# Performance work log

Measured on AMD Instinct MI355X. Metric: run time of the kernel, lower is better.

## Reference

```python
import jax, jax.numpy as jnp
import numpy as np

B, T, DIM, HEADS, DH, MLP = 2, 1024, 768, 8, 96, 3072
EPS = 1e-6


def _rms_norm(x, w):
    return x * jax.lax.rsqrt(jnp.mean(x * x, axis=-1, keepdims=True) + EPS) * w


def _rotate_half(x):
    x1, x2 = jnp.split(x, 2, axis=-1)
    return jnp.concatenate([-x2, x1], axis=-1)


def _l2norm(x):
    n = jnp.sqrt(jnp.sum(x * x, axis=-1, keepdims=True))
    return x / jnp.maximum(n, 1e-12)


def setup_inputs() -> dict:
    key = jax.random.key(0)
    ks = jax.random.split(key, 16)
    def rn(k, shape, s=0.02):
        return jax.random.normal(k, shape, jnp.float32) * s
    return {
        'x_stream1': jax.random.normal(ks[0], (B, T, DIM), jnp.float32),
        'x_stream2': jax.random.normal(ks[1], (B, T, DIM), jnp.float32),
        'p_emb': jax.random.normal(ks[2], (B, 1, 1024), jnp.float32),
        'mod_w1': rn(ks[3], (1024, 512)), 'mod_b1': jnp.zeros((512,), jnp.float32),
        'mod_w2': rn(ks[4], (512, DIM * 12)), 'mod_b2': jnp.zeros((DIM * 12,), jnp.float32),
        'norm11_w': jnp.ones((DIM,), jnp.float32), 'norm12_w': jnp.ones((DIM,), jnp.float32),
        'qkv_w': rn(ks[5], (DIM, 3 * DIM)), 'qkv_b': jnp.zeros((3 * DIM,), jnp.float32),
        'qkv2_w': rn(ks[6], (DIM, 3 * DIM)), 'qkv2_b': jnp.zeros((3 * DIM,), jnp.float32),
        'qk_scale': jnp.full((DH,), 10.0, jnp.float32),
        'out_w': rn(ks[7], (DIM, DIM)), 'out_b': jnp.zeros((DIM,), jnp.float32),
        'norm21_w': jnp.ones((DIM,), jnp.float32), 'norm22_w': jnp.ones((DIM,), jnp.float32),
        'mlp1_w1': rn(ks[8], (DIM, MLP)), 'mlp1_b1': jnp.zeros((MLP,), jnp.float32),
        'mlp1_w2': rn(ks[9], (MLP, DIM)), 'mlp1_b2': jnp.zeros((DIM,), jnp.float32),
        'mlp2_w1': rn(ks[10], (DIM, MLP)), 'mlp2_b1': jnp.zeros((MLP,), jnp.float32),
        'mlp2_w2': rn(ks[11], (MLP, DIM)), 'mlp2_b2': jnp.zeros((DIM,), jnp.float32),
    }


def _forward(x_stream1, x_stream2, p_emb, mod_w1, mod_b1, mod_w2, mod_b2,
             norm11_w, norm12_w, qkv_w, qkv_b, qkv2_w, qkv2_b, qk_scale,
             out_w, out_b, norm21_w, norm22_w,
             mlp1_w1, mlp1_b1, mlp1_w2, mlp1_b2,
             mlp2_w1, mlp2_b1, mlp2_w2, mlp2_b2):
    Bc, Tc, D = x_stream1.shape
    # modulation MLP: SiLU -> Linear -> SiLU -> Linear -> 12 chunks of [B, D]
    h = jax.nn.silu(p_emb[:, 0, :])
    h = jax.nn.silu(h @ mod_w1 + mod_b1)
    mod = h @ mod_w2 + mod_b2
    (m1s, m1h, m1g, m2s, m2h, m2g,
     m3s, m3h, m3g, m4s, m4h, m4g) = [m[:, None, :] for m in jnp.split(mod, 12, axis=1)]

    xm1 = _rms_norm(x_stream1, norm11_w) * (1 + m1s) + m1h
    xm2 = _rms_norm(x_stream2, norm12_w) * (1 + m2s) + m2h

    q1, k1, v1 = jnp.split(xm1 @ qkv_w + qkv_b, 3, axis=-1)
    q2, k2, v2 = jnp.split(xm2 @ qkv2_w + qkv2_b, 3, axis=-1)
    q = jnp.concatenate([q1, q2], axis=1)  # [B, 2T, D]
    k = jnp.concatenate([k1, k2], axis=1)
    v = jnp.concatenate([v1, v2], axis=1)
    N = 2 * Tc

    def to_heads(x):
        return x.reshape(Bc, N, HEADS, DH).transpose(0, 2, 1, 3)  # [B, H, N, dh]
    q, k, v = to_heads(q), to_heads(k), to_heads(v)

    # RoPE (inv_freq computed in bf16 as in the original, then used in fp32)
    inv_freq = (1.0 / (10000.0 ** (jnp.arange(0, DH, 2, dtype=jnp.float32) / DH))).astype(jnp.bfloat16).astype(jnp.float32)
    t = jnp.arange(N, dtype=jnp.float32)
    freqs = t[:, None] * inv_freq[None, :]
    emb = jnp.concatenate([freqs, freqs], axis=-1)  # [N, dh]
    cos, sin = jnp.cos(emb), jnp.sin(emb)
    q = q * cos + _rotate_half(q) * sin
    k = k * cos + _rotate_half(k) * sin

    # QK-Norm
    q = _l2norm(q) * qk_scale
    k = _l2norm(k) * qk_scale

    scores = jnp.einsum('bhid,bhjd->bhij', q, k) * (DH ** -0.5)
    probs = jax.nn.softmax(scores, axis=-1)
    attn = jnp.einsum('bhij,bhjd->bhid', probs, v)
    attn = attn.transpose(0, 2, 1, 3).reshape(Bc, N, D)
    attn = attn @ out_w + out_b

    x1 = x_stream1 + attn[:, :Tc, :] * m1g
    x2 = x_stream2 + attn[:, Tc:, :] * m2g

    xn1 = _rms_norm(x1, norm21_w) * (1 + m3s) + m3h
    mlp1 = jax.nn.gelu(xn1 @ mlp1_w1 + mlp1_b1, approximate=False) @ mlp1_w2 + mlp1_b2
    xn2 = _rms_norm(x2, norm22_w) * (1 + m4s) + m4h
    mlp2 = jax.nn.gelu(xn2 @ mlp2_w1 + mlp2_b1, approximate=False) @ mlp2_w2 + mlp2_b2

    return (x1 + mlp1 * m3g, x2 + mlp2 * m4g)


def reference(x_stream1, x_stream2, p_emb, mod_w1, mod_b1, mod_w2, mod_b2,
              norm11_w, norm12_w, qkv_w, qkv_b, qkv2_w, qkv2_b, qk_scale,
              out_w, out_b, norm21_w, norm22_w,
              mlp1_w1, mlp1_b1, mlp1_w2, mlp1_b2,
              mlp2_w1, mlp2_b1, mlp2_w2, mlp2_b2):
    return _forward(x_stream1, x_stream2, p_emb, mod_w1, mod_b1, mod_w2, mod_b2,
                    norm11_w, norm12_w, qkv_w, qkv_b, qkv2_w, qkv2_b, qk_scale,
                    out_w, out_b, norm21_w, norm22_w,
                    mlp1_w1, mlp1_b1, mlp1_w2, mlp1_b2,
                    mlp2_w1, mlp2_b1, mlp2_w2, mlp2_b2)
```

## Files before the change

### kernel.cpp

```cpp
#include <hip/hip_runtime.h>
#include <hip/hip_bf16.h>
#include <cstdint>
#include <math.h>

#define BB 2
#define TT 1024
#define DIMM 768
#define NHEADS 8
#define DHH 96
#define MLPD 3072
#define NN 2048

typedef unsigned short u16;
using short8 = __attribute__((ext_vector_type(8))) short;
using f32x4  = __attribute__((ext_vector_type(4))) float;
using f32x16 = __attribute__((ext_vector_type(16))) float;
using int4v  = __attribute__((ext_vector_type(4))) int;
union S8I4 { int4v i; short8 s; };

static constexpr float kEps = 1e-6f;

__device__ __forceinline__ float siluf(float x){ return x / (1.f + expf(-x)); }
__device__ __forceinline__ float geluf(float x){ return 0.5f*x*(1.f + erff(x*0.7071067811865475f)); }
__device__ __forceinline__ float bf16_rne(float x){
  uint32_t u = __float_as_uint(x);
  u = (u + 0x7fffu + ((u >> 16) & 1u)) & 0xffff0000u;
  return __uint_as_float(u);
}
__device__ __forceinline__ u16 f2b(float x){
  uint32_t u = __float_as_uint(x);
  return (u16)((u + 0x7fffu + ((u >> 16) & 1u)) >> 16);
}
__device__ __forceinline__ float b2f(u16 b){
  return __uint_as_float(((uint32_t)b) << 16);
}
__device__ __forceinline__ int cvtpk(float lo, float hi){
  int d; asm("v_cvt_pk_bf16_f32 %0, %1, %2" : "=v"(d) : "v"(lo), "v"(hi)); return d;
}
__device__ __forceinline__ void gload16(const void* g, void* l){
  __builtin_amdgcn_global_load_lds((const __attribute__((address_space(1))) unsigned int*)g,
                                   (__attribute__((address_space(3))) unsigned int*)l, 16, 0, 0);
}

__global__ __launch_bounds__(256) void mod_stage1_k(
    const float* __restrict__ p_emb, const float* __restrict__ w1,
    const float* __restrict__ b1, float* __restrict__ h2){
  __shared__ float sp[1024];
  const int b = blockIdx.x >> 1;
  const int obase = (blockIdx.x & 1) * 256;
  for (int i = threadIdx.x; i < 1024; i += 256)
    sp[i] = siluf(p_emb[b*1024 + i]);
  __syncthreads();
  const int o = obase + threadIdx.x;
  float acc = 0.f;
  for (int j = 0; j < 1024; ++j) acc += sp[j] * w1[j*512 + o];
  h2[b*512 + o] = siluf(acc + b1[o]);
}

__global__ __launch_bounds__(256) void mod_stage2_k(
    const float* __restrict__ h2, const float* __restrict__ w2,
    const float* __restrict__ b2, float* __restrict__ mod){
  __shared__ float sh[512];
  const int b = blockIdx.x / 36;
  const int obase = (blockIdx.x % 36) * 256;
  for (int i = threadIdx.x; i < 512; i += 256)
    sh[i] = h2[b*512 + i];
  __syncthreads();
  const int o = obase + threadIdx.x;
  float acc = 0.f;
  for (int j = 0; j < 512; ++j) acc += sh[j] * w2[j*9216 + o];
  mod[b*9216 + o] = acc + b2[o];
}

__global__ __launch_bounds__(256) void wt_all_k(
    const float* __restrict__ s0, u16* __restrict__ d0,
    const float* __restrict__ s1, u16* __restrict__ d1,
    const float* __restrict__ s2, u16* __restrict__ d2,
    const float* __restrict__ s3, u16* __restrict__ d3,
    const float* __restrict__ s4, u16* __restrict__ d4,
    const float* __restrict__ s5, u16* __restrict__ d5,
    const float* __restrict__ s6, u16* __restrict__ d6){
  const int bid = blockIdx.x;
  const float* S; u16* D; int K, N, lid;
  if      (bid < 1728) { S=s0; D=d0; K=768;  N=2304; lid=bid; }
  else if (bid < 3456) { S=s1; D=d1; K=768;  N=2304; lid=bid-1728; }
  else if (bid < 4032) { S=s2; D=d2; K=768;  N=768;  lid=bid-3456; }
  else if (bid < 6336) { S=s3; D=d3; K=768;  N=3072; lid=bid-4032; }
  else if (bid < 8640) { S=s4; D=d4; K=3072; N=768;  lid=bid-6336; }
  else if (bid < 10944){ S=s5; D=d5; K=768;  N=3072; lid=bid-8640; }
  else                 { S=s6; D=d6; K=3072; N=768;  lid=bid-10944; }
  const int nx = N >> 5;
  const int k0 = (lid / nx) * 32, n0 = (lid % nx) * 32;
  __shared__ float t[32][33];
  const int tx = threadIdx.x & 31, ty = threadIdx.x >> 5;
  for (int i = ty; i < 32; i += 8)
    t[i][tx] = S[(size_t)(k0+i)*N + n0 + tx];
  __syncthreads();
  for (int i = ty; i < 32; i += 8)
    D[(size_t)(n0+i)*K + k0 + tx] = f2b(t[tx][i]);
}

__global__ __launch_bounds__(256) void rmsnorm2_k(
    const float* __restrict__ x0, const float* __restrict__ w0, int cs0, int ch0, u16* __restrict__ o0,
    const float* __restrict__ x1, const float* __restrict__ w1, int cs1, int ch1, u16* __restrict__ o1,
    const float* __restrict__ mod){
  const int rowg = blockIdx.x;
  const int s = rowg >> 11;
  const int row = rowg & 2047;
  const float* x = s ? x1 : x0;
  const float* w = s ? w1 : w0;
  const int cs = s ? cs1 : cs0, ch = s ? ch1 : ch0;
  u16* out = s ? o1 : o0;
  const int b = row >> 10;
  const int tid = threadIdx.x;
  const float* xr = x + (size_t)row * DIMM;
  float v0 = xr[tid], v1 = xr[tid + 256], v2 = xr[tid + 512];
  float ss = v0*v0 + v1*v1 + v2*v2;
  __shared__ float red[4];
  for (int m = 1; m < 64; m <<= 1) ss += __shfl_xor(ss, m, 64);
  if ((tid & 63) == 0) red[tid >> 6] = ss;
  __syncthreads();
  float tot = red[0] + red[1] + red[2] + red[3];
  float rms = rsqrtf(tot * (1.f/768.f) + kEps);
  const float* ms = mod + (size_t)b*9216 + (size_t)cs*768;
  const float* mh = mod + (size_t)b*9216 + (size_t)ch*768;
  u16* orow = out + (size_t)row * DIMM;
  orow[tid]       = f2b(v0*rms*w[tid]      *(1.f+ms[tid])       + mh[tid]);
  orow[tid + 256] = f2b(v1*rms*w[tid+256]  *(1.f+ms[tid+256])   + mh[tid+256]);
  orow[tid + 512] = f2b(v2*rms*w[tid+512]  *(1.f+ms[tid+512])   + mh[tid+512]);
}

template<int EPI, int DUAL>
__global__ __launch_bounds__(256) void gemm_pipe_k(
    const u16* __restrict__ A0, const u16* __restrict__ Bt0,
    const float* __restrict__ bias0, void* __restrict__ C0,
    const u16* __restrict__ A1, const u16* __restrict__ Bt1,
    const float* __restrict__ bias1, void* __restrict__ C1,
    int M, int N, int K){
  __shared__ u16 As[3][128*32];
  __shared__ u16 Bs[3][128*32];
  const int z = DUAL ? blockIdx.z : 0;
  const u16* A      = z ? A1 : A0;
  const u16* Bt     = z ? Bt1 : Bt0;
  const float* bias = z ? bias1 : bias0;
  void* C           = z ? C1 : C0;
  const int tid = threadIdx.x;
  const int w = tid >> 6, l = tid & 63;
  const int m0 = blockIdx.y*128, n0 = blockIdx.x*128;
  const int wr = w >> 1, wc = w & 1;
  const int la = l & 15, hi4 = l >> 4;
  f32x4 acc[4][4] = {};
  const int nk = K >> 5;
  const int sb0 = w*128, sb1 = w*128 + 64;
  const int s0i = sb0 + l, s1i = sb1 + l;
  const int r0 = s0i >> 2, c0 = ((s0i & 3) ^ ((r0 >> 1) & 3)) * 8;
  const int r1 = s1i >> 2, c1 = ((s1i & 3) ^ ((r1 >> 1) & 3)) * 8;
  const u16* Ar0 = A  + (size_t)(m0+r0)*K + c0;
  const u16* Ar1 = A  + (size_t)(m0+r1)*K + c1;
  const u16* Br0 = Bt + (size_t)(n0+r0)*K + c0;
  const u16* Br1 = Bt + (size_t)(n0+r1)*K + c1;
  #define STAGE(buf, kofs) { \
    gload16(Ar0 + (kofs), &As[buf][sb0*8]); \
    gload16(Br0 + (kofs), &Bs[buf][sb0*8]); \
    gload16(Ar1 + (kofs), &As[buf][sb1*8]); \
    gload16(Br1 + (kofs), &Bs[buf][sb1*8]); }
  STAGE(0, 0);
  STAGE(1, 32);
  const int rslot = ((hi4 ^ ((l >> 1) & 3)) << 4);
  int cur = 0;
  for (int kt = 0; kt < nk; ++kt){
    if (kt + 1 < nk){ asm volatile("s_waitcnt vmcnt(4)" ::: "memory"); }
    else            { asm volatile("s_waitcnt vmcnt(0)" ::: "memory"); }
    __builtin_amdgcn_s_barrier();
    if (kt + 2 < nk){
      int nb = cur + 2; if (nb >= 3) nb -= 3;
      STAGE(nb, (kt+2) << 5);
    }
    short8 af[4], bf[4];
    #pragma unroll
    for (int mi = 0; mi < 4; ++mi)
      af[mi] = *(const short8*)((const char*)&As[cur][0] + (wr*64 + mi*16 + la)*64 + rslot);
    #pragma unroll
    for (int ni = 0; ni < 4; ++ni)
      bf[ni] = *(const short8*)((const char*)&Bs[cur][0] + (wc*64 + ni*16 + la)*64 + rslot);
    #pragma unroll
    for (int mi = 0; mi < 4; ++mi)
      #pragma unroll
      for (int ni = 0; ni < 4; ++ni)
        acc[mi][ni] = __builtin_amdgcn_mfma_f32_16x16x32_bf16(af[mi], bf[ni], acc[mi][ni], 0, 0, 0);
    if (++cur == 3) cur = 0;
  }
  #undef STAGE
  #pragma unroll
  for (int mi = 0; mi < 4; ++mi){
    #pragma unroll
    for (int ni = 0; ni < 4; ++ni){
      const int n = n0 + wc*64 + ni*16 + la;
      const float bv = bias[n];
      #pragma unroll
      for (int rr = 0; rr < 4; ++rr){
        const int m = m0 + wr*64 + mi*16 + hi4*4 + rr;
        float v = acc[mi][ni][rr] + bv;
        if constexpr (EPI == 2) v = geluf(v);
        ((u16*)C)[(size_t)m*N + n] = f2b(v);
      }
    }
  }
}

template<int EPI, int DUAL>
__global__ __launch_bounds__(1024) void gemm16_k(
    const u16* __restrict__ A0, const u16* __restrict__ Bt0,
    const float* __restrict__ bias0,
    const u16* __restrict__ A1, const u16* __restrict__ Bt1,
    const float* __restrict__ bias1,
    const float* __restrict__ mod, const float* __restrict__ X0,
    const float* __restrict__ X1, float* __restrict__ O0,
    float* __restrict__ O1, int cg0, int cg1,
    int M, int N, int K){
  __shared__ char lds[131072];
  const int bid = blockIdx.x;
  const int xcd = bid & 7, kk = bid >> 3;
  const int g = xcd + 8*(kk/6);
  const int x = kk % 6;
  int by, z;
  if constexpr (DUAL){ by = g & 15; z = g >> 4; } else { by = g; z = 0; }
  const u16* A      = z ? A1 : A0;
  const u16* Bt     = z ? Bt1 : Bt0;
  const float* bias = z ? bias1 : bias0;
  const int tid = threadIdx.x;
  const int w = tid >> 6, l = tid & 63;
  const int kg = w >> 2, gw = w & 3;
  const int m0 = by*128, n0 = x*128;
  const int wr = gw >> 1, wc = gw & 1;
  const int la = l & 15, hi4 = l >> 4;
  u16* AsG = (u16*)(lds + kg*32768);
  u16* BsG = (u16*)(lds + kg*32768 + 16384);
  const int Kg = K >> 2;
  const int nk = Kg >> 5;
  const int kbase = kg * Kg;
  f32x4 acc[4][4] = {};
  #pragma unroll
  for (int it = 0; it < 2; ++it){
    const int sb = gw*128 + it*64;
    const int s = sb + l;
    const int row = s >> 2, scol = ((s & 3) ^ ((row >> 1) & 3)) * 8;
    gload16(A  + (size_t)(m0+row)*K + kbase + scol, AsG + sb*8);
    gload16(Bt + (size_t)(n0+row)*K + kbase + scol, BsG + sb*8);
  }
  __syncthreads();
  const int rslot = (hi4 ^ ((l >> 1) & 3)) * 8;
  for (int kt = 0; kt < nk; ++kt){
    const int cur = kt & 1;
    if (kt + 1 < nk){
      const int k0n = kbase + ((kt+1) << 5);
      #pragma unroll
      for (int it = 0; it < 2; ++it){
        const int sb = gw*128 + it*64;
        const int s = sb + l;
        const int row = s >> 2, scol = ((s & 3) ^ ((row >> 1) & 3)) * 8;
        gload16(A  + (size_t)(m0+row)*K + k0n + scol, AsG + (cur^1)*4096 + sb*8);
        gload16(Bt + (size_t)(n0+row)*K + k0n + scol, BsG + (cur^1)*4096 + sb*8);
      }
    }
    short8 af[4], bf[4];
    #pragma unroll
    for (int mi = 0; mi < 4; ++mi)
      af[mi] = *(const short8*)(AsG + cur*4096 + (wr*64 + mi*16 + la)*32 + rslot);
    #pragma unroll
    for (int ni = 0; ni < 4; ++ni)
      bf[ni] = *(const short8*)(BsG + cur*4096 + (wc*64 + ni*16 + la)*32 + rslot);
    #pragma unroll
    for (int mi = 0; mi < 4; ++mi)
      #pragma unroll
      for (int ni = 0; ni < 4; ++ni)
        acc[mi][ni] = __builtin_amdgcn_mfma_f32_16x16x32_bf16(af[mi], bf[ni], acc[mi][ni], 0, 0, 0);
    __syncthreads();
  }
  float* c0 = (float*)lds;
  float* c1 = (float*)(lds + 65536);
  #define WRACC(cb) { \
    _Pragma("unroll") for (int mi = 0; mi < 4; ++mi) \
    _Pragma("unroll") for (int ni = 0; ni < 4; ++ni) \
    _Pragma("unroll") for (int rr = 0; rr < 4; ++rr) \
      (cb)[(wr*64+mi*16+hi4*4+rr)*128 + wc*64+ni*16+la] = acc[mi][ni][rr]; }
  #define RDACC(cb) { \
    _Pragma("unroll") for (int mi = 0; mi < 4; ++mi) \
    _Pragma("unroll") for (int ni = 0; ni < 4; ++ni) \
    _Pragma("unroll") for (int rr = 0; rr < 4; ++rr) \
      acc[mi][ni][rr] += (cb)[(wr*64+mi*16+hi4*4+rr)*128 + wc*64+ni*16+la]; }
  if (kg == 1) WRACC(c0);
  if (kg == 3) WRACC(c1);
  __syncthreads();
  if (kg == 0) RDACC(c0);
  if (kg == 2) RDACC(c1);
  __syncthreads();
  if (kg == 2) WRACC(c0);
  __syncthreads();
  if (kg == 0){
    RDACC(c0);
    #pragma unroll
    for (int mi = 0; mi < 4; ++mi){
      #pragma unroll
      for (int ni = 0; ni < 4; ++ni){
        const int n = n0 + wc*64 + ni*16 + la;
        const float bv = bias[n];
        #pragma unroll
        for (int rr = 0; rr < 4; ++rr){
          const int m = m0 + wr*64 + mi*16 + hi4*4 + rr;
          float v = acc[mi][ni][rr] + bv;
          if constexpr (EPI == 3){
            const int bb = m >> 11, ss = (m >> 10) & 1, t = m & 1023;
            const float* X = ss ? X1 : X0;
            float* O = ss ? O1 : O0;
            const float gmod = mod[(size_t)bb*9216 + (size_t)(ss ? cg1 : cg0)*768 + n];
            const size_t oi = ((size_t)(bb*1024 + t))*768 + n;
            O[oi] = X[oi] + v*gmod;
          } else {
            float* O = z ? O1 : O0;
            const int cg = z ? cg1 : cg0;
            const int bb = m >> 10;
            const float gmod = mod[(size_t)bb*9216 + (size_t)cg*768 + n];
            O[(size_t)m*N + n] += v*gmod;
          }
        }
      }
    }
  }
  #undef WRACC
  #undef RDACC
}

__global__ __launch_bounds__(256) void build_qkv_k(
    const u16* __restrict__ qkv1, const u16* __restrict__ qkv2,
    const float* __restrict__ qk_scale,
    u16* __restrict__ Q, u16* __restrict__ K, u16* __restrict__ V){
  const int wid = threadIdx.x >> 6;
  const int lane = threadIdx.x & 63;
  const int row = blockIdx.x * 4 + wid;
  const int n = row & 2047;
  const int h = (row >> 11) & 7;
  const int b = row >> 14;
  const u16* src = (n < TT) ? (qkv1 + ((size_t)b*TT + n) * 2304)
                            : (qkv2 + ((size_t)b*TT + (n - TT)) * 2304);
  const int col = h * DHH;
  const bool act = lane < 48;
  float q0=0,q1=0,k0=0,k1=0,v0=0,v1=0,c=1.f,s=0.f,sc0=0,sc1=0;
  if (act){
    q0 = b2f(src[col + lane]);        q1 = b2f(src[col + lane + 48]);
    k0 = b2f(src[768 + col + lane]);  k1 = b2f(src[768 + col + lane + 48]);
    v0 = b2f(src[1536 + col + lane]); v1 = b2f(src[1536 + col + lane + 48]);
    float inv = bf16_rne((float)(1.0 / pow(10000.0, (2.0 * lane) / 96.0)));
    float ang = (float)n * inv;
    c = cosf(ang); s = sinf(ang);
    sc0 = qk_scale[lane]; sc1 = qk_scale[lane + 48];
  }
  float qr0 = q0*c - q1*s, qr1 = q1*c + q0*s;
  float kr0 = k0*c - k1*s, kr1 = k1*c + k0*s;
  float ssq = qr0*qr0 + qr1*qr1;
  float ssk = kr0*kr0 + kr1*kr1;
  for (int m = 1; m < 64; m <<= 1){ ssq += __shfl_xor(ssq, m, 64); ssk += __shfl_xor(ssk, m, 64); }
  float rq = 1.f / fmaxf(sqrtf(ssq), 1e-12f);
  float rk = 1.f / fmaxf(sqrtf(ssk), 1e-12f);
  const float sscale = 0.1020620726159658f;
  if (act){
    size_t base = (size_t)row * DHH;
    Q[base + lane]      = f2b(qr0*rq*sc0*sscale);  Q[base + lane + 48] = f2b(qr1*rq*sc1*sscale);
    K[base + lane]      = f2b(kr0*rk*sc0);         K[base + lane + 48] = f2b(kr1*rk*sc1);
    V[base + lane]      = f2b(v0);                 V[base + lane + 48] = f2b(v1);
  }
}

__global__ __launch_bounds__(256) void vtrans_k(
    const u16* __restrict__ Vtmp, u16* __restrict__ Vt){
  __shared__ u16 t[32][33];
  const int bh = blockIdx.z;
  const int n0 = blockIdx.x*32, d0 = blockIdx.y*32;
  const int tx = threadIdx.x & 31, ty = threadIdx.x >> 5;
  for (int i = ty; i < 32; i += 8)
    t[i][tx] = Vtmp[((size_t)bh*NN + n0+i)*DHH + d0 + tx];
  __syncthreads();
  for (int i = ty; i < 32; i += 8)
    Vt[((size_t)bh*DHH + d0+i)*NN + n0 + tx] = t[tx][i];
}

#define CROW(r) (((r)&3) + 8*((r)>>2) + 4*hi)
#define SMAXC 10.5f
#define BUILD_PA(dst, vec, basei) { \
  int a1_ = cvtpk(vec[basei+0], vec[basei+1]); \
  int b1_ = cvtpk(vec[basei+4], vec[basei+5]); \
  asm("v_permlane32_swap_b32 %0, %1" : "+v"(a1_), "+v"(b1_)); \
  int a2_ = cvtpk(vec[basei+2], vec[basei+3]); \
  int b2_ = cvtpk(vec[basei+6], vec[basei+7]); \
  asm("v_permlane32_swap_b32 %0, %1" : "+v"(a2_), "+v"(b2_)); \
  S8I4 u_; u_.i = (int4v){a1_, a2_, b1_, b2_}; dst = u_.s; }

__global__ __launch_bounds__(512) void attn_mfma_k(
    const u16* __restrict__ Qg, const u16* __restrict__ Kg,
    const u16* __restrict__ Vtg, u16* __restrict__ AO){
  __shared__ u16 Ks[2][2][64*128];
  __shared__ u16 Vs[2][2][96*64];
  const int bh = blockIdx.x >> 4;
  const int qblk = blockIdx.x & 15;
  const int b = bh >> 3, h = bh & 7;
  const int tid = threadIdx.x;
  const int w = tid >> 6, l = tid & 63;
  const int g2 = w >> 2, wq = w & 3;
  const int gtid = tid & 255;
  const int hi = l >> 5, li = l & 31;
  const int q0w = qblk*128 + wq*32;
  const int kvbase = g2 * 1024;

  short8 qf[6];
  {
    const u16* qrow = Qg + ((size_t)bh*NN + q0w + li)*DHH;
    #pragma unroll
    for (int ks = 0; ks < 6; ++ks)
      qf[ks] = *(const short8*)(qrow + ks*16 + hi*8);
  }

  f32x16 o0, o1, o2;
  #pragma unroll
  for (int r = 0; r < 16; ++r){ o0[r]=0.f; o1[r]=0.f; o2[r]=0.f; }
  float lrun = 0.f;

  {
    #pragma unroll
    for (int it = 0; it < 3; ++it){
      const int s = gtid + it*256;
      const int krow = s/12, ksl = s%12;
      short8 kv = *(const short8*)(Kg + ((size_t)bh*NN + kvbase + krow)*DHH + ksl*8);
      *(short8*)((char*)&Ks[g2][0][0] + krow*256 + ((ksl ^ (krow&7))<<4)) = kv;
      const int vrow = s >> 3, vsl = s & 7;
      short8 vv = *(const short8*)(Vtg + ((size_t)bh*DHH + vrow)*NN + kvbase + vsl*8);
      *(short8*)((char*)&Vs[g2][0][0] + vrow*128 + ((vsl ^ (vrow&7))<<4)) = vv;
    }
  }
  __syncthreads();

  const int NT2 = 16;
  for (int t = 0; t < NT2; ++t){
    const int cur = t & 1;
    short8 kst[3], vst[3];
    if (t + 1 < NT2){
      const int kv0 = kvbase + (t+1)*64;
      #pragma unroll
      for (int it = 0; it < 3; ++it){
        const int s = gtid + it*256;
        const int krow = s/12, ksl = s%12;
        kst[it] = *(const short8*)(Kg + ((size_t)bh*NN + kv0 + krow)*DHH + ksl*8);
        const int vrow = s >> 3, vsl = s & 7;
        vst[it] = *(const short8*)(Vtg + ((size_t)bh*DHH + vrow)*NN + kv0 + vsl*8);
      }
    }
    f32x16 s0, s1;
    #pragma unroll
    for (int r = 0; r < 16; ++r){ s0[r]=0.f; s1[r]=0.f; }
    #pragma unroll
    for (int ks = 0; ks < 6; ++ks){
      const int sl = ks*2 + hi;
      short8 kf0 = *(const short8*)((const char*)&Ks[g2][cur][0] + li*256      + ((sl ^ (li&7))<<4));
      short8 kf1 = *(const short8*)((const char*)&Ks[g2][cur][0] + (32+li)*256 + ((sl ^ ((32+li)&7))<<4));
      s0 = __builtin_amdgcn_mfma_f32_32x32x16_bf16(kf0, qf[ks], s0, 0, 0, 0);
      s1 = __builtin_amdgcn_mfma_f32_32x32x16_bf16(kf1, qf[ks], s1, 0, 0, 0);
    }
    float ps = 0.f;
    #pragma unroll
    for (int r = 0; r < 16; ++r){
      float pa = __expf(s0[r] - SMAXC);
      float pb = __expf(s1[r] - SMAXC);
      s0[r] = pa; s1[r] = pb; ps += pa + pb;
    }
    ps += __shfl_xor(ps, 32);
    lrun += ps;
    short8 pa0, pa1, pa2, pa3;
    BUILD_PA(pa0, s0, 0); BUILD_PA(pa1, s0, 8);
    BUILD_PA(pa2, s1, 0); BUILD_PA(pa3, s1, 8);
    #pragma unroll
    for (int dt = 0; dt < 3; ++dt){
      const int drow = dt*32 + li;
      const char* vb_base = (const char*)&Vs[g2][cur][0] + drow*128;
      f32x16* op = (dt==0)? &o0 : (dt==1)? &o1 : &o2;
      {
        short8 vb = *(const short8*)(vb_base + (((0*2+hi) ^ (drow&7))<<4));
        *op = __builtin_amdgcn_mfma_f32_32x32x16_bf16(pa0, vb, *op, 0, 0, 0);
      }
      {
        short8 vb = *(const short8*)(vb_base + (((1*2+hi) ^ (drow&7))<<4));
        *op = __builtin_amdgcn_mfma_f32_32x32x16_bf16(pa1, vb, *op, 0, 0, 0);
      }
      {
        short8 vb = *(const short8*)(vb_base + (((2*2+hi) ^ (drow&7))<<4));
        *op = __builtin_amdgcn_mfma_f32_32x32x16_bf16(pa2, vb, *op, 0, 0, 0);
      }
      {
        short8 vb = *(const short8*)(vb_base + (((3*2+hi) ^ (drow&7))<<4));
        *op = __builtin_amdgcn_mfma_f32_32x32x16_bf16(pa3, vb, *op, 0, 0, 0);
      }
    }
    __syncthreads();
    if (t + 1 < NT2){
      #pragma unroll
      for (int it = 0; it < 3; ++it){
        const int s = gtid + it*256;
        const int krow = s/12, ksl = s%12;
        *(short8*)((char*)&Ks[g2][cur^1][0] + krow*256 + ((ksl ^ (krow&7))<<4)) = kst[it];
        const int vrow = s >> 3, vsl = s & 7;
        *(short8*)((char*)&Vs[g2][cur^1][0] + vrow*128 + ((vsl ^ (vrow&7))<<4)) = vst[it];
      }
      __syncthreads();
    }
  }

  float* cmb = (float*)&Ks[0][0][0];
  float* cl  = (float*)&Vs[0][0][0];
  if (g2 == 1){
    #pragma unroll
    for (int r = 0; r < 16; ++r){
      cmb[((wq*16 + r)*3 + 0)*64 + l] = o0[r];
      cmb[((wq*16 + r)*3 + 1)*64 + l] = o1[r];
      cmb[((wq*16 + r)*3 + 2)*64 + l] = o2[r];
    }
    if (l < 32) cl[wq*32 + l] = lrun;
  }
  __syncthreads();
  if (g2 == 0){
    #pragma unroll
    for (int r = 0; r < 16; ++r){
      o0[r] += cmb[((wq*16 + r)*3 + 0)*64 + l];
      o1[r] += cmb[((wq*16 + r)*3 + 1)*64 + l];
      o2[r] += cmb[((wq*16 + r)*3 + 2)*64 + l];
    }
    lrun += cl[wq*32 + li];
    const float linv = 1.f / lrun;
    #pragma unroll
    for (int r = 0; r < 16; ++r){
      const float lr = __shfl(linv, CROW(r), 64);
      const int n = q0w + CROW(r);
      u16* dst = AO + ((size_t)b*NN + n)*DIMM + h*DHH + li;
      dst[0]  = f2b(o0[r]*lr);
      dst[32] = f2b(o1[r]*lr);
      dst[64] = f2b(o2[r]*lr);
    }
  }
}

static constexpr size_t W_QKV1T = 0;
static constexpr size_t W_QKV2T = W_QKV1T + 3538944;
static constexpr size_t W_OUTT  = W_QKV2T + 3538944;
static constexpr size_t W_M1W1T = W_OUTT  + 1179648;
static constexpr size_t W_M1W2T = W_M1W1T + 4718592;
static constexpr size_t W_M2W1T = W_M1W2T + 4718592;
static constexpr size_t W_M2W2T = W_M2W1T + 4718592;
static constexpr size_t O_MODH  = W_M2W2T + 4718592;
static constexpr size_t O_MODB  = O_MODH + 4096;
static constexpr size_t DYN     = O_MODB + 73728;
static constexpr size_t O_XM1   = DYN;
static constexpr size_t O_XM2   = O_XM1 + 3145728;
static constexpr size_t O_QKV1  = O_XM2 + 3145728;
static constexpr size_t O_QKV2  = O_QKV1 + 9437184;
static constexpr size_t O_QB    = O_QKV2 + 9437184;
static constexpr size_t O_KB    = O_QB + 6291456;
static constexpr size_t O_VTMP  = O_KB + 6291456;
static constexpr size_t O_PF    = O_VTMP + 6291456;
static constexpr size_t O_VT    = O_QKV1;
static constexpr size_t O_AO    = O_QKV2;
static constexpr size_t O_H1    = O_QB;
static constexpr size_t O_H2    = O_PF;

extern "C" void kernel_launch(void* const* d_in, const int* in_sizes, int n_in,
                              void* d_out, int out_size, void* d_ws, size_t ws_size,
                              hipStream_t stream){
  const float* x_s1   = (const float*)d_in[0];
  const float* x_s2   = (const float*)d_in[1];
  const float* p_emb  = (const float*)d_in[2];
  const float* mod_w1 = (const float*)d_in[3];
  const float* mod_b1 = (const float*)d_in[4];
  const float* mod_w2 = (const float*)d_in[5];
  const float* mod_b2 = (const float*)d_in[6];
  const float* n11_w  = (const float*)d_in[7];
  const float* n12_w  = (const float*)d_in[8];
  const float* qkv_w  = (const float*)d_in[9];
  const float* qkv_b  = (const float*)d_in[10];
  const float* qkv2_w = (const float*)d_in[11];
  const float* qkv2_b = (const float*)d_in[12];
  const float* qk_sc  = (const float*)d_in[13];
  const float* out_w  = (const float*)d_in[14];
  const float* out_b  = (const float*)d_in[15];
  const float* n21_w  = (const float*)d_in[16];
  const float* n22_w  = (const float*)d_in[17];
  const float* m1w1   = (const float*)d_in[18];
  const float* m1b1   = (const float*)d_in[19];
  const float* m1w2   = (const float*)d_in[20];
  const float* m1b2   = (const float*)d_in[21];
  const float* m2w1   = (const float*)d_in[22];
  const float* m2b1   = (const float*)d_in[23];
  const float* m2w2   = (const float*)d_in[24];
  const float* m2b2   = (const float*)d_in[25];

  char* ws = (char*)d_ws;
  u16* qkv1t = (u16*)(ws + W_QKV1T);
  u16* qkv2t = (u16*)(ws + W_QKV2T);
  u16* outt  = (u16*)(ws + W_OUTT);
  u16* w11t  = (u16*)(ws + W_M1W1T);
  u16* w12t  = (u16*)(ws + W_M1W2T);
  u16* w21t  = (u16*)(ws + W_M2W1T);
  u16* w22t  = (u16*)(ws + W_M2W2T);
  float* h2b  = (float*)(ws + O_MODH);
  float* modb = (float*)(ws + O_MODB);
  u16* xm1  = (u16*)(ws + O_XM1);
  u16* xm2  = (u16*)(ws + O_XM2);
  u16* qkv1 = (u16*)(ws + O_QKV1);
  u16* qkv2 = (u16*)(ws + O_QKV2);
  u16* Qb   = (u16*)(ws + O_QB);
  u16* Kb   = (u16*)(ws + O_KB);
  u16* Vtmp = (u16*)(ws + O_VTMP);
  u16* Vt   = (u16*)(ws + O_VT);
  u16* AO   = (u16*)(ws + O_AO);
  u16* H1   = (u16*)(ws + O_H1);
  u16* H2   = (u16*)(ws + O_H2);

  float* out0 = (float*)d_out;
  float* out1 = out0 + (size_t)BB*TT*DIMM;

  wt_all_k<<<13248, 256, 0, stream>>>(qkv_w, qkv1t, qkv2_w, qkv2t, out_w, outt,
                                      m1w1, w11t, m1w2, w12t, m2w1, w21t, m2w2, w22t);

  mod_stage1_k<<<4, 256, 0, stream>>>(p_emb, mod_w1, mod_b1, h2b);
  mod_stage2_k<<<72, 256, 0, stream>>>(h2b, mod_w2, mod_b2, modb);

  rmsnorm2_k<<<2*BB*TT, 256, 0, stream>>>(x_s1, n11_w, 0, 1, xm1,
                                          x_s2, n12_w, 3, 4, xm2, modb);

  gemm_pipe_k<1,1><<<dim3(18, 16, 2), 256, 0, stream>>>(
      xm1, qkv1t, qkv_b, qkv1, xm2, qkv2t, qkv2_b, qkv2, 2048, 2304, 768);

  build_qkv_k<<<(BB*NHEADS*NN)/4, 256, 0, stream>>>(qkv1, qkv2, qk_sc, Qb, Kb, Vtmp);

  vtrans_k<<<dim3(NN/32, DHH/32, 16), 256, 0, stream>>>(Vtmp, Vt);

  attn_mfma_k<<<16*16, 512, 0, stream>>>(Qb, Kb, Vt, AO);

  gemm16_k<3,0><<<192, 1024, 0, stream>>>(
      AO, outt, out_b, AO, outt, out_b,
      modb, x_s1, x_s2, out0, out1, 2, 5, 4096, 768, 768);

  rmsnorm2_k<<<2*BB*TT, 256, 0, stream>>>(out0, n21_w, 6, 7, xm1,
                                          out1, n22_w, 9, 10, xm2, modb);

  gemm_pipe_k<2,1><<<dim3(24, 16, 2), 256, 0, stream>>>(
      xm1, w11t, m1b1, H1, xm2, w21t, m2b1, H2, 2048, 3072, 768);

  gemm16_k<4,1><<<192, 1024, 0, stream>>>(
      H1, w12t, m1b2, H2, w22t, m2b2,
      modb, nullptr, nullptr, out0, out1, 8, 11, 2048, 768, 3072);
}
```

Baseline: 281.0 us.

## Enlarge QKV and MLP-up GEMM tiles to 256x256 with 512 threads

Replaces the 128x128 triple-buffered GEMM with a 256x256-tile, 512-thread kernel using BK=64, double buffering, an 8-way XOR LDS swizzle and s_setprio around the MFMA bursts. Bigger tiles raise arithmetic intensity and cut global reloads of A and B. In exchange the grid shrinks to 144 and 192 blocks on a GPU with 256 CUs, so fewer CUs are busy. LDS use reaches 128KB, which allows only one block per CU. The single wait-then-barrier per k-step also exposes more load latency.

After: 342.1 us. +21.8%, slower.

```diff
diff --git a/kernel.cpp b/kernel.cpp
--- a/kernel.cpp
+++ b/kernel.cpp
@@ -131,14 +131,14 @@
 }
 
 template<int EPI, int DUAL>
-__global__ __launch_bounds__(256) void gemm_pipe_k(
+__global__ __launch_bounds__(512, 1) void gemm256_k(
     const u16* __restrict__ A0, const u16* __restrict__ Bt0,
     const float* __restrict__ bias0, void* __restrict__ C0,
     const u16* __restrict__ A1, const u16* __restrict__ Bt1,
     const float* __restrict__ bias1, void* __restrict__ C1,
     int M, int N, int K){
-  __shared__ u16 As[3][128*32];
-  __shared__ u16 Bs[3][128*32];
+  __shared__ u16 As[2][256*64];
+  __shared__ u16 Bs[2][256*64];
   const int z = DUAL ? blockIdx.z : 0;
   const u16* A      = z ? A1 : A0;
   const u16* Bt     = z ? Bt1 : Bt0;
@@ -146,60 +146,79 @@
   void* C           = z ? C1 : C0;
   const int tid = threadIdx.x;
   const int w = tid >> 6, l = tid & 63;
-  const int m0 = blockIdx.y*128, n0 = blockIdx.x*128;
-  const int wr = w >> 1, wc = w & 1;
+  const int m0 = blockIdx.y*256, n0 = blockIdx.x*256;
+  const int wr = w >> 2, wc = w & 3;
   const int la = l & 15, hi4 = l >> 4;
-  f32x4 acc[4][4] = {};
-  const int nk = K >> 5;
-  const int sb0 = w*128, sb1 = w*128 + 64;
-  const int s0i = sb0 + l, s1i = sb1 + l;
-  const int r0 = s0i >> 2, c0 = ((s0i & 3) ^ ((r0 >> 1) & 3)) * 8;
-  const int r1 = s1i >> 2, c1 = ((s1i & 3) ^ ((r1 >> 1) & 3)) * 8;
-  const u16* Ar0 = A  + (size_t)(m0+r0)*K + c0;
-  const u16* Ar1 = A  + (size_t)(m0+r1)*K + c1;
-  const u16* Br0 = Bt + (size_t)(n0+r0)*K + c0;
-  const u16* Br1 = Bt + (size_t)(n0+r1)*K + c1;
+  f32x4 acc[8][4] = {};
+  const int nt = K >> 6;
+  const int sA0 = tid, sA1 = tid + 512, sA2 = tid + 1024, sA3 = tid + 1536;
+  #define MKP(si) \
+    const int r_##si = (si) >> 3; \
+    const int c_##si = (((si) & 7) ^ (r_##si & 7)) * 8;
+  MKP(sA0) MKP(sA1) MKP(sA2) MKP(sA3)
+  const u16* Ap0 = A  + (size_t)(m0+r_sA0)*K + c_sA0;
+  const u16* Ap1 = A  + (size_t)(m0+r_sA1)*K + c_sA1;
+  const u16* Ap2 = A  + (size_t)(m0+r_sA2)*K + c_sA2;
+  const u16* Ap3 = A  + (size_t)(m0+r_sA3)*K + c_sA3;
+  const u16* Bp0 = Bt + (size_t)(n0+r_sA0)*K + c_sA0;
+  const u16* Bp1 = Bt + (size_t)(n0+r_sA1)*K + c_sA1;
+  const u16* Bp2 = Bt + (size_t)(n0+r_sA2)*K + c_sA2;
+  const u16* Bp3 = Bt + (size_t)(n0+r_sA3)*K + c_sA3;
+  #undef MKP
   #define STAGE(buf, kofs) { \
-    gload16(Ar0 + (kofs), &As[buf][sb0*8]); \
-    gload16(Br0 + (kofs), &Bs[buf][sb0*8]); \
-    gload16(Ar1 + (kofs), &As[buf][sb1*8]); \
-    gload16(Br1 + (kofs), &Bs[buf][sb1*8]); }
+    gload16(Ap0 + (kofs), &As[buf][sA0*8]); \
+    gload16(Bp0 + (kofs), &Bs[buf][sA0*8]); \
+    gload16(Ap1 + (kofs), &As[buf][sA1*8]); \
+    gload16(Bp1 + (kofs), &Bs[buf][sA1*8]); \
+    gload16(Ap2 + (kofs), &As[buf][sA2*8]); \
+    gload16(Bp2 + (kofs), &Bs[buf][sA2*8]); \
+    gload16(Ap3 + (kofs), &As[buf][sA3*8]); \
+    gload16(Bp3 + (kofs), &Bs[buf][sA3*8]); }
   STAGE(0, 0);
-  STAGE(1, 32);
-  const int rslot = ((hi4 ^ ((l >> 1) & 3)) << 4);
+  asm volatile("s_waitcnt vmcnt(0)" ::: "memory");
+  __builtin_amdgcn_s_barrier();
   int cur = 0;
-  for (int kt = 0; kt < nk; ++kt){
-    if (kt + 1 < nk){ asm volatile("s_waitcnt vmcnt(4)" ::: "memory"); }
-    else            { asm volatile("s_waitcnt vmcnt(0)" ::: "memory"); }
-    __builtin_amdgcn_s_barrier();
-    if (kt + 2 < nk){
-      int nb = cur + 2; if (nb >= 3) nb -= 3;
-      STAGE(nb, (kt+2) << 5);
-    }
-    short8 af[4], bf[4];
-    #pragma unroll
-    for (int mi = 0; mi < 4; ++mi)
-      af[mi] = *(const short8*)((const char*)&As[cur][0] + (wr*64 + mi*16 + la)*64 + rslot);
-    #pragma unroll
-    for (int ni = 0; ni < 4; ++ni)
-      bf[ni] = *(const short8*)((const char*)&Bs[cur][0] + (wc*64 + ni*16 + la)*64 + rslot);
-    #pragma unroll
-    for (int mi = 0; mi < 4; ++mi)
-      #pragma unroll
-      for (int ni = 0; ni < 4; ++ni)
-        acc[mi][ni] = __builtin_amdgcn_mfma_f32_16x16x32_bf16(af[mi], bf[ni], acc[mi][ni], 0, 0, 0);
-    if (++cur == 3) cur = 0;
+  for (int kt = 0; kt < nt; ++kt){
+    if (kt + 1 < nt) STAGE(cur^1, (kt+1) << 6);
+    #pragma unroll
+    for (int ks2 = 0; ks2 < 2; ++ks2){
+      short8 af[8], bf[4];
+      #pragma unroll
+      for (int mi = 0; mi < 8; ++mi){
+        const int row = wr*128 + mi*16 + la;
+        const int slot = (ks2*4 + hi4) ^ (row & 7);
+        af[mi] = *(const short8*)(&As[cur][row*64 + slot*8]);
+      }
+      #pragma unroll
+      for (int ni = 0; ni < 4; ++ni){
+        const int row = wc*64 + ni*16 + la;
+        const int slot = (ks2*4 + hi4) ^ (row & 7);
+        bf[ni] = *(const short8*)(&Bs[cur][row*64 + slot*8]);
+      }
+      __builtin_amdgcn_s_setprio(1);
+      #pragma unroll
+      for (int mi = 0; mi < 8; ++mi)
+        #pragma unroll
+        for (int ni = 0; ni < 4; ++ni)
+          acc[mi][ni] = __builtin_amdgcn_mfma_f32_16x16x32_bf16(af[mi], bf[ni], acc[mi][ni], 0, 0, 0);
+      __builtin_amdgcn_s_setprio(0);
+    }
+    if (kt + 1 < nt){
+      asm volatile("s_waitcnt vmcnt(0)" ::: "memory");
+      __builtin_amdgcn_s_barrier();
+      cur ^= 1;
+    }
   }
   #undef STAGE
   #pragma unroll
-  for (int mi = 0; mi < 4; ++mi){
+  for (int mi = 0; mi < 8; ++mi){
     #pragma unroll
     for (int ni = 0; ni < 4; ++ni){
       const int n = n0 + wc*64 + ni*16 + la;
       const float bv = bias[n];
       #pragma unroll
       for (int rr = 0; rr < 4; ++rr){
-        const int m = m0 + wr*64 + mi*16 + hi4*4 + rr;
+        const int m = m0 + wr*128 + mi*16 + hi4*4 + rr;
         float v = acc[mi][ni][rr] + bv;
         if constexpr (EPI == 2) v = geluf(v);
         ((u16*)C)[(size_t)m*N + n] = f2b(v);
@@ -632,7 +651,7 @@
   rmsnorm2_k<<<2*BB*TT, 256, 0, stream>>>(x_s1, n11_w, 0, 1, xm1,
                                           x_s2, n12_w, 3, 4, xm2, modb);
 
-  gemm_pipe_k<1,1><<<dim3(18, 16, 2), 256, 0, stream>>>(
+  gemm256_k<1,1><<<dim3(9, 8, 2), 512, 0, stream>>>(
       xm1, qkv1t, qkv_b, qkv1, xm2, qkv2t, qkv2_b, qkv2, 2048, 2304, 768);
 
   build_qkv_k<<<(BB*NHEADS*NN)/4, 256, 0, stream>>>(qkv1, qkv2, qk_sc, Qb, Kb, Vtmp);
@@ -648,7 +667,7 @@
   rmsnorm2_k<<<2*BB*TT, 256, 0, stream>>>(out0, n21_w, 6, 7, xm1,
                                           out1, n22_w, 9, 10, xm2, modb);
 
-  gemm_pipe_k<2,1><<<dim3(24, 16, 2), 256, 0, stream>>>(
+  gemm256_k<2,1><<<dim3(12, 8, 2), 512, 0, stream>>>(
       xm1, w11t, m1b1, H1, xm2, w21t, m2b1, H2, 2048, 3072, 768);
 
   gemm16_k<4,1><<<192, 1024, 0, stream>>>(
```

## Replace 128x128 pipelined GEMM with 256x256 8-wave ping-pong GEMM

Applied to the files above, without the earlier changes.

The QKV and MLP-up GEMMs now use 256x256 tiles with 512 threads, each wave computing 128x64, and a double-buffered K=64 stage. Loads are split into half-stages interleaved with MFMA phases under explicit scheduling barriers and s_setprio. The aim is more operand reuse per LDS byte and better overlap of global loads with MFMA work. The cost is far fewer blocks (144 and 192 for 256 CUs), which risks leaving CUs idle, plus higher register and LDS use per block.

Result: slower. 343.0 us (+22.0%).

```diff
diff --git a/kernel.cpp b/kernel.cpp
--- a/kernel.cpp
+++ b/kernel.cpp
@@ -130,15 +130,16 @@
   orow[tid + 512] = f2b(v2*rms*w[tid+512]  *(1.f+ms[tid+512])   + mh[tid+512]);
 }
 
+#define SBAR { __builtin_amdgcn_sched_barrier(0); __builtin_amdgcn_s_barrier(); __builtin_amdgcn_sched_barrier(0); }
 template<int EPI, int DUAL>
-__global__ __launch_bounds__(256) void gemm_pipe_k(
+__global__ __launch_bounds__(512, 1) void gemm8p_k(
     const u16* __restrict__ A0, const u16* __restrict__ Bt0,
     const float* __restrict__ bias0, void* __restrict__ C0,
     const u16* __restrict__ A1, const u16* __restrict__ Bt1,
     const float* __restrict__ bias1, void* __restrict__ C1,
     int M, int N, int K){
-  __shared__ u16 As[3][128*32];
-  __shared__ u16 Bs[3][128*32];
+  __shared__ u16 As[2][2][256*32];
+  __shared__ u16 Bs[2][2][256*32];
   const int z = DUAL ? blockIdx.z : 0;
   const u16* A      = z ? A1 : A0;
   const u16* Bt     = z ? Bt1 : Bt0;
@@ -146,60 +147,109 @@
   void* C           = z ? C1 : C0;
   const int tid = threadIdx.x;
   const int w = tid >> 6, l = tid & 63;
-  const int m0 = blockIdx.y*128, n0 = blockIdx.x*128;
-  const int wr = w >> 1, wc = w & 1;
+  const int m0 = blockIdx.y*256, n0 = blockIdx.x*256;
+  const int wr = w >> 2, wc = w & 3;
   const int la = l & 15, hi4 = l >> 4;
-  f32x4 acc[4][4] = {};
-  const int nk = K >> 5;
-  const int sb0 = w*128, sb1 = w*128 + 64;
-  const int s0i = sb0 + l, s1i = sb1 + l;
-  const int r0 = s0i >> 2, c0 = ((s0i & 3) ^ ((r0 >> 1) & 3)) * 8;
-  const int r1 = s1i >> 2, c1 = ((s1i & 3) ^ ((r1 >> 1) & 3)) * 8;
-  const u16* Ar0 = A  + (size_t)(m0+r0)*K + c0;
-  const u16* Ar1 = A  + (size_t)(m0+r1)*K + c1;
-  const u16* Br0 = Bt + (size_t)(n0+r0)*K + c0;
-  const u16* Br1 = Bt + (size_t)(n0+r1)*K + c1;
-  #define STAGE(buf, kofs) { \
-    gload16(Ar0 + (kofs), &As[buf][sb0*8]); \
-    gload16(Br0 + (kofs), &Bs[buf][sb0*8]); \
-    gload16(Ar1 + (kofs), &As[buf][sb1*8]); \
-    gload16(Br1 + (kofs), &Bs[buf][sb1*8]); }
-  STAGE(0, 0);
-  STAGE(1, 32);
-  const int rslot = ((hi4 ^ ((l >> 1) & 3)) << 4);
-  int cur = 0;
-  for (int kt = 0; kt < nk; ++kt){
-    if (kt + 1 < nk){ asm volatile("s_waitcnt vmcnt(4)" ::: "memory"); }
-    else            { asm volatile("s_waitcnt vmcnt(0)" ::: "memory"); }
-    __builtin_amdgcn_s_barrier();
-    if (kt + 2 < nk){
-      int nb = cur + 2; if (nb >= 3) nb -= 3;
-      STAGE(nb, (kt+2) << 5);
-    }
+  f32x4 acc[8][4] = {};
+  const int nt = K >> 6;
+  const int u0 = tid, u1 = tid + 512;
+  const int r0 = u0 >> 2, c0 = ((u0 & 3) ^ (r0 & 3)) * 8;
+  const int r1 = u1 >> 2, c1 = ((u1 & 3) ^ (r1 & 3)) * 8;
+  const u16* Agr0 = A  + (size_t)(m0 + r0)*K + c0;
+  const u16* Agr1 = A  + (size_t)(m0 + r1)*K + c1;
+  const u16* Bgr0 = Bt + (size_t)(n0 + r0)*K + c0;
+  const u16* Bgr1 = Bt + (size_t)(n0 + r1)*K + c1;
+  #define STG_A(buf, kh, kof) { \
+    gload16(Agr0 + (kof) + (kh)*32, &As[buf][kh][u0*8]); \
+    gload16(Agr1 + (kof) + (kh)*32, &As[buf][kh][u1*8]); }
+  #define STG_B(buf, kh, kof) { \
+    gload16(Bgr0 + (kof) + (kh)*32, &Bs[buf][kh][u0*8]); \
+    gload16(Bgr1 + (kof) + (kh)*32, &Bs[buf][kh][u1*8]); }
+  #define RD_A(dst, buf, kh, mi_) { \
+    const int row_ = wr*128 + (mi_)*16 + la; \
+    dst = *(const short8*)(&As[buf][kh][row_*32 + (hi4 ^ (row_ & 3))*8]); }
+  #define RD_B(dst, buf, kh, ni_) { \
+    const int row_ = wc*64 + (ni_)*16 + la; \
+    dst = *(const short8*)(&Bs[buf][kh][row_*32 + (hi4 ^ (row_ & 3))*8]); }
+  STG_A(0, 0, 0); STG_B(0, 0, 0); STG_A(0, 1, 0); STG_B(0, 1, 0);
+  asm volatile("s_waitcnt vmcnt(4)" ::: "memory");
+  SBAR;
+  for (int kt = 0; kt < nt; ++kt){
+    const int cb = kt & 1, nb = cb ^ 1;
+    const bool pre = (kt + 1 < nt);
+    const int kof = (kt + 1) << 6;
     short8 af[4], bf[4];
     #pragma unroll
-    for (int mi = 0; mi < 4; ++mi)
-      af[mi] = *(const short8*)((const char*)&As[cur][0] + (wr*64 + mi*16 + la)*64 + rslot);
-    #pragma unroll
-    for (int ni = 0; ni < 4; ++ni)
-      bf[ni] = *(const short8*)((const char*)&Bs[cur][0] + (wc*64 + ni*16 + la)*64 + rslot);
+    for (int i = 0; i < 4; ++i) RD_A(af[i], cb, 0, i);
+    #pragma unroll
+    for (int i = 0; i < 4; ++i) RD_B(bf[i], cb, 0, i);
+    if (pre) STG_A(nb, 0, kof);
+    SBAR;
+    __builtin_amdgcn_s_setprio(1);
     #pragma unroll
     for (int mi = 0; mi < 4; ++mi)
       #pragma unroll
       for (int ni = 0; ni < 4; ++ni)
         acc[mi][ni] = __builtin_amdgcn_mfma_f32_16x16x32_bf16(af[mi], bf[ni], acc[mi][ni], 0, 0, 0);
-    if (++cur == 3) cur = 0;
-  }
-  #undef STAGE
+    __builtin_amdgcn_s_setprio(0);
+    SBAR;
+    #pragma unroll
+    for (int i = 0; i < 4; ++i) RD_A(af[i], cb, 0, 4 + i);
+    if (pre) STG_B(nb, 0, kof);
+    if (pre){ asm volatile("s_waitcnt vmcnt(4)" ::: "memory"); }
+    else    { asm volatile("s_waitcnt vmcnt(0)" ::: "memory"); }
+    SBAR;
+    __builtin_amdgcn_s_setprio(1);
+    #pragma unroll
+    for (int mi = 0; mi < 4; ++mi)
+      #pragma unroll
+      for (int ni = 0; ni < 4; ++ni)
+        acc[4 + mi][ni] = __builtin_amdgcn_mfma_f32_16x16x32_bf16(af[mi], bf[ni], acc[4 + mi][ni], 0, 0, 0);
+    __builtin_amdgcn_s_setprio(0);
+    SBAR;
+    #pragma unroll
+    for (int i = 0; i < 4; ++i) RD_A(af[i], cb, 1, i);
+    #pragma unroll
+    for (int i = 0; i < 4; ++i) RD_B(bf[i], cb, 1, i);
+    if (pre) STG_A(nb, 1, kof);
+    SBAR;
+    __builtin_amdgcn_s_setprio(1);
+    #pragma unroll
+    for (int mi = 0; mi < 4; ++mi)
+      #pragma unroll
+      for (int ni = 0; ni < 4; ++ni)
+        acc[mi][ni] = __builtin_amdgcn_mfma_f32_16x16x32_bf16(af[mi], bf[ni], acc[mi][ni], 0, 0, 0);
+    __builtin_amdgcn_s_setprio(0);
+    SBAR;
+    #pragma unroll
+    for (int i = 0; i < 4; ++i) RD_A(af[i], cb, 1, 4 + i);
+    if (pre){
+      STG_B(nb, 1, kof);
+      asm volatile("s_waitcnt vmcnt(4)" ::: "memory");
+    }
+    SBAR;
+    __builtin_amdgcn_s_setprio(1);
+    #pragma unroll
+    for (int mi = 0; mi < 4; ++mi)
+      #pragma unroll
+      for (int ni = 0; ni < 4; ++ni)
+        acc[4 + mi][ni] = __builtin_amdgcn_mfma_f32_16x16x32_bf16(af[mi], bf[ni], acc[4 + mi][ni], 0, 0, 0);
+    __builtin_amdgcn_s_setprio(0);
+    SBAR;
+  }
+  #undef STG_A
+  #undef STG_B
+  #undef RD_A
+  #undef RD_B
   #pragma unroll
-  for (int mi = 0; mi < 4; ++mi){
+  for (int mi = 0; mi < 8; ++mi){
     #pragma unroll
     for (int ni = 0; ni < 4; ++ni){
       const int n = n0 + wc*64 + ni*16 + la;
       const float bv = bias[n];
       #pragma unroll
       for (int rr = 0; rr < 4; ++rr){
-        const int m = m0 + wr*64 + mi*16 + hi4*4 + rr;
+        const int m = m0 + wr*128 + mi*16 + hi4*4 + rr;
         float v = acc[mi][ni][rr] + bv;
         if constexpr (EPI == 2) v = geluf(v);
         ((u16*)C)[(size_t)m*N + n] = f2b(v);
@@ -632,7 +682,7 @@
   rmsnorm2_k<<<2*BB*TT, 256, 0, stream>>>(x_s1, n11_w, 0, 1, xm1,
                                           x_s2, n12_w, 3, 4, xm2, modb);
 
-  gemm_pipe_k<1,1><<<dim3(18, 16, 2), 256, 0, stream>>>(
+  gemm8p_k<1,1><<<dim3(9, 8, 2), 512, 0, stream>>>(
       xm1, qkv1t, qkv_b, qkv1, xm2, qkv2t, qkv2_b, qkv2, 2048, 2304, 768);
 
   build_qkv_k<<<(BB*NHEADS*NN)/4, 256, 0, stream>>>(qkv1, qkv2, qk_sc, Qb, Kb, Vtmp);
@@ -648,7 +698,7 @@
   rmsnorm2_k<<<2*BB*TT, 256, 0, stream>>>(out0, n21_w, 6, 7, xm1,
                                           out1, n22_w, 9, 10, xm2, modb);
 
-  gemm_pipe_k<2,1><<<dim3(24, 16, 2), 256, 0, stream>>>(
+  gemm8p_k<2,1><<<dim3(12, 8, 2), 512, 0, stream>>>(
       xm1, w11t, m1b1, H1, xm2, w21t, m2b1, H2, 2048, 3072, 768);
 
   gemm16_k<4,1><<<192, 1024, 0, stream>>>(
```

## Replace LDS-staged GEMM with register-direct per-wave loads for QKV and MLP-up

Applied to the files above, without the earlier changes.

Swaps the shared-memory triple-buffered GEMM for a version where each wave loads its MFMA operand fragments straight from global memory into registers, double-buffered in registers, with tiles reshaped to 256x64 per block. This removes the LDS staging, barriers and swizzle overhead. In exchange, B-tile data is no longer shared across waves, so global and L2 traffic goes up, and the 16-byte per-lane loads are strided by K rather than coalesced.

Result: slower. 358.8 us (+27.7%).

```diff
diff --git a/kernel.cpp b/kernel.cpp
--- a/kernel.cpp
+++ b/kernel.cpp
@@ -131,14 +131,12 @@
 }
 
 template<int EPI, int DUAL>
-__global__ __launch_bounds__(256) void gemm_pipe_k(
+__global__ __launch_bounds__(256) void gemm_wv_k(
     const u16* __restrict__ A0, const u16* __restrict__ Bt0,
     const float* __restrict__ bias0, void* __restrict__ C0,
     const u16* __restrict__ A1, const u16* __restrict__ Bt1,
     const float* __restrict__ bias1, void* __restrict__ C1,
     int M, int N, int K){
-  __shared__ u16 As[3][128*32];
-  __shared__ u16 Bs[3][128*32];
   const int z = DUAL ? blockIdx.z : 0;
   const u16* A      = z ? A1 : A0;
   const u16* Bt     = z ? Bt1 : Bt0;
@@ -146,60 +144,42 @@
   void* C           = z ? C1 : C0;
   const int tid = threadIdx.x;
   const int w = tid >> 6, l = tid & 63;
-  const int m0 = blockIdx.y*128, n0 = blockIdx.x*128;
-  const int wr = w >> 1, wc = w & 1;
   const int la = l & 15, hi4 = l >> 4;
+  const int m_off = blockIdx.y*256 + w*64;
+  const int n_off = blockIdx.x*64;
+  const u16* Ab = A  + (size_t)(m_off + la)*K + hi4*8;
+  const u16* Bb = Bt + (size_t)(n_off + la)*K + hi4*8;
   f32x4 acc[4][4] = {};
   const int nk = K >> 5;
-  const int sb0 = w*128, sb1 = w*128 + 64;
-  const int s0i = sb0 + l, s1i = sb1 + l;
-  const int r0 = s0i >> 2, c0 = ((s0i & 3) ^ ((r0 >> 1) & 3)) * 8;
-  const int r1 = s1i >> 2, c1 = ((s1i & 3) ^ ((r1 >> 1) & 3)) * 8;
-  const u16* Ar0 = A  + (size_t)(m0+r0)*K + c0;
-  const u16* Ar1 = A  + (size_t)(m0+r1)*K + c1;
-  const u16* Br0 = Bt + (size_t)(n0+r0)*K + c0;
-  const u16* Br1 = Bt + (size_t)(n0+r1)*K + c1;
-  #define STAGE(buf, kofs) { \
-    gload16(Ar0 + (kofs), &As[buf][sb0*8]); \
-    gload16(Br0 + (kofs), &Bs[buf][sb0*8]); \
-    gload16(Ar1 + (kofs), &As[buf][sb1*8]); \
-    gload16(Br1 + (kofs), &Bs[buf][sb1*8]); }
-  STAGE(0, 0);
-  STAGE(1, 32);
-  const int rslot = ((hi4 ^ ((l >> 1) & 3)) << 4);
-  int cur = 0;
-  for (int kt = 0; kt < nk; ++kt){
-    if (kt + 1 < nk){ asm volatile("s_waitcnt vmcnt(4)" ::: "memory"); }
-    else            { asm volatile("s_waitcnt vmcnt(0)" ::: "memory"); }
-    __builtin_amdgcn_s_barrier();
-    if (kt + 2 < nk){
-      int nb = cur + 2; if (nb >= 3) nb -= 3;
-      STAGE(nb, (kt+2) << 5);
-    }
-    short8 af[4], bf[4];
-    #pragma unroll
-    for (int mi = 0; mi < 4; ++mi)
-      af[mi] = *(const short8*)((const char*)&As[cur][0] + (wr*64 + mi*16 + la)*64 + rslot);
-    #pragma unroll
-    for (int ni = 0; ni < 4; ++ni)
-      bf[ni] = *(const short8*)((const char*)&Bs[cur][0] + (wc*64 + ni*16 + la)*64 + rslot);
-    #pragma unroll
-    for (int mi = 0; mi < 4; ++mi)
-      #pragma unroll
-      for (int ni = 0; ni < 4; ++ni)
-        acc[mi][ni] = __builtin_amdgcn_mfma_f32_16x16x32_bf16(af[mi], bf[ni], acc[mi][ni], 0, 0, 0);
-    if (++cur == 3) cur = 0;
-  }
-  #undef STAGE
+  short8 aX[4], bX[4], aY[4], bY[4];
+  #define LDAB(adst, bdst, kof) { \
+    _Pragma("unroll") for (int i = 0; i < 4; ++i) \
+      adst[i] = *(const short8*)(Ab + (size_t)i*16*K + (kof)); \
+    _Pragma("unroll") for (int i = 0; i < 4; ++i) \
+      bdst[i] = *(const short8*)(Bb + (size_t)i*16*K + (kof)); }
+  #define MM(a_, b_) { \
+    _Pragma("unroll") for (int mi = 0; mi < 4; ++mi) \
+    _Pragma("unroll") for (int ni = 0; ni < 4; ++ni) \
+      acc[mi][ni] = __builtin_amdgcn_mfma_f32_16x16x32_bf16(a_[mi], b_[ni], acc[mi][ni], 0, 0, 0); }
+  LDAB(aX, bX, 0);
+  LDAB(aY, bY, 32);
+  for (int kt = 0; kt < nk; kt += 2){
+    MM(aX, bX);
+    if (kt + 2 < nk) LDAB(aX, bX, (size_t)(kt+2)*32);
+    if (kt + 1 < nk) MM(aY, bY);
+    if (kt + 3 < nk) LDAB(aY, bY, (size_t)(kt+3)*32);
+  }
+  #undef LDAB
+  #undef MM
   #pragma unroll
   for (int mi = 0; mi < 4; ++mi){
     #pragma unroll
     for (int ni = 0; ni < 4; ++ni){
-      const int n = n0 + wc*64 + ni*16 + la;
+      const int n = n_off + ni*16 + la;
       const float bv = bias[n];
       #pragma unroll
       for (int rr = 0; rr < 4; ++rr){
-        const int m = m0 + wr*64 + mi*16 + hi4*4 + rr;
+        const int m = m_off + mi*16 + hi4*4 + rr;
         float v = acc[mi][ni][rr] + bv;
         if constexpr (EPI == 2) v = geluf(v);
         ((u16*)C)[(size_t)m*N + n] = f2b(v);
@@ -632,7 +612,7 @@
   rmsnorm2_k<<<2*BB*TT, 256, 0, stream>>>(x_s1, n11_w, 0, 1, xm1,
                                           x_s2, n12_w, 3, 4, xm2, modb);
 
-  gemm_pipe_k<1,1><<<dim3(18, 16, 2), 256, 0, stream>>>(
+  gemm_wv_k<1,1><<<dim3(36, 8, 2), 256, 0, stream>>>(
       xm1, qkv1t, qkv_b, qkv1, xm2, qkv2t, qkv2_b, qkv2, 2048, 2304, 768);
 
   build_qkv_k<<<(BB*NHEADS*NN)/4, 256, 0, stream>>>(qkv1, qkv2, qk_sc, Qb, Kb, Vtmp);
@@ -648,7 +628,7 @@
   rmsnorm2_k<<<2*BB*TT, 256, 0, stream>>>(out0, n21_w, 6, 7, xm1,
                                           out1, n22_w, 9, 10, xm2, modb);
 
-  gemm_pipe_k<2,1><<<dim3(24, 16, 2), 256, 0, stream>>>(
+  gemm_wv_k<2,1><<<dim3(48, 8, 2), 256, 0, stream>>>(
       xm1, w11t, m1b1, H1, xm2, w21t, m2b1, H2, 2048, 3072, 768);
 
   gemm16_k<4,1><<<192, 1024, 0, stream>>>(
```
